# Kernel tuning notes

Measured on AMD Instinct MI355X. Metric: run time of the kernel, lower is better.

Reference implementation:

```python
import jax, jax.numpy as jnp
import numpy as np

UNITS = 256
INNER_ITERS = 1
INNER_LR = [0.01]
LN_EPS = 1e-3  # keras LayerNormalization default epsilon
B, L, F = 512, 128, 128


def _encoder(W1, b1, W2, b2, z):
    # keras 'gelu' activation is exact (approximate=False)
    h = jax.nn.gelu(z @ W1 + b1, approximate=False)
    return h @ W2 + b2


def _layer_norm(z, g, b):
    m = jnp.mean(z, axis=-1, keepdims=True)
    v = jnp.var(z, axis=-1, keepdims=True)
    return g * (z - m) / jnp.sqrt(v + LN_EPS) + b


def setup_inputs():
    U = UNITS
    key = jax.random.key(0)
    ks = jax.random.split(key, 12)
    s = 0.02
    return {
        "inputs": jax.random.normal(ks[0], (B, F), jnp.float32),
        "prev_hidden": jax.random.normal(ks[1], (B, U), jnp.float32),
        "sequence_buffer": jax.random.normal(ks[2], (B, L, U), jnp.float32),
        "Wp": jax.random.normal(ks[3], (F, U)) * s, "bp": jnp.zeros((U,)),
        "Wphi": jax.random.normal(ks[4], (U, U)) * s, "bphi": jnp.zeros((U,)),
        "Wpsi": jax.random.normal(ks[5], (U, U)) * s, "bpsi": jnp.zeros((U,)),
        "W1": jax.random.normal(ks[6], (U, 4 * U)) * s, "b1": jnp.zeros((4 * U,)),
        "W2": jax.random.normal(ks[7], (4 * U, U)) * s, "b2": jnp.zeros((U,)),
        "Wg": jax.random.normal(ks[8], (U, U)) * s, "g_bias": jnp.zeros((U,)),
        "ln_g": jnp.ones((U,)), "ln_b": jnp.zeros((U,)),
        "Wh": jax.random.normal(ks[9], (U, U)) * s, "h_bias": jnp.zeros((U,)),
    }


def reference(inputs, prev_hidden, sequence_buffer, Wp, bp, Wphi, bphi, Wpsi, bpsi,
              W1, b1, W2, b2, Wg, g_bias, ln_g, ln_b, Wh, h_bias):
    U = UNITS
    bsz = inputs.shape[0]
    # input projection (F != units)
    proj = inputs @ Wp + bp                                   # [B, U]
    # shift buffer, append projected input
    buf = jnp.concatenate([sequence_buffer[:, 1:, :], proj[:, None, :]], axis=1)  # [B, L, U]
    x = buf[:, :-1, :].reshape(-1, U)                         # [B*(L-1), U]
    y = buf[:, 1:, :].reshape(-1, U)
    phi = x @ Wphi + bphi

    params = (W1, b1, W2, b2)

    def inner_loss(p):
        rec = _layer_norm(_encoder(*p, phi) @ Wg + g_bias, ln_g, ln_b)
        return jnp.mean(jnp.square(rec - y)), rec

    rec = None
    for it in range(INNER_ITERS):
        (_, rec), grads = jax.value_and_grad(inner_loss, has_aux=True)(params)
        lr = INNER_LR[min(it, len(INNER_LR) - 1)]
        params = tuple(p - lr * g for p, g in zip(params, grads))

    psi = buf[:, -1, :] @ Wpsi + bpsi                         # [B, U]
    contrib = jnp.mean(rec.reshape(bsz, -1, U), axis=1)       # [B, U]
    # psi path uses the UPDATED inner-encoder weights
    out = (_encoder(*params, psi) + contrib) @ Wh + h_bias    # [B, U]
    return out, buf
```

## Files before the change

### kernel.cpp

```cpp
#include <hip/hip_runtime.h>
#include <cmath>

typedef __bf16 bf16;
typedef __attribute__((ext_vector_type(8))) __bf16 bf16x8;
typedef __attribute__((ext_vector_type(4))) __bf16 bf16x4v;
typedef __attribute__((ext_vector_type(4))) float f32x4;
typedef __attribute__((ext_vector_type(2))) unsigned int u32x2;

constexpr int NROWS = 512 * 127;
constexpr float LR = 0.01f;
constexpr float INV_NU = 1.f / (65024.f * 256.f);

__device__ __forceinline__ float sigf(float x) {
  return 1.f / (1.f + __expf(-1.702f * x));
}
__device__ __forceinline__ float gelu_fast(float x) { return x * sigf(x); }
__device__ __forceinline__ float dgelu_fast(float x) {
  float s = sigf(x);
  return s * (1.f + 1.702f * x * (1.f - s));
}
__device__ __forceinline__ bf16x8 gelu8f(bf16x8 v) {
  bf16x8 o;
#pragma unroll
  for (int i = 0; i < 8; i++) o[i] = (bf16)gelu_fast((float)v[i]);
  return o;
}

__device__ __forceinline__ void gload16(const bf16* g, const bf16* lds) {
  __builtin_amdgcn_global_load_lds(
      (const __attribute__((address_space(1))) unsigned int*)(size_t)(const void*)g,
      (__attribute__((address_space(3))) unsigned int*)(unsigned)(size_t)(const void*)lds,
      16, 0, 0);
}

__device__ __forceinline__ int xcd_lin() {
  int p = ((int)blockIdx.z * (int)gridDim.y + (int)blockIdx.y) * (int)gridDim.x + (int)blockIdx.x;
  const int total = (int)gridDim.x * (int)gridDim.y * (int)gridDim.z;
  if (!(total & 7)) p = (p & 7) * (total >> 3) + (p >> 3);
  return p;
}

template <int EPI>
__global__ __launch_bounds__(256) void gemm3_k(
    const bf16* __restrict__ A, const bf16* __restrict__ Bt,
    const float* __restrict__ bias, void* __restrict__ out0,
    void* __restrict__ out1, const bf16* __restrict__ aux,
    int M, int N, int K) {
  __shared__ __align__(16) bf16 As[2][128 * 64];
  __shared__ __align__(16) bf16 Bs[2][128 * 64];
  const int t = threadIdx.x;
  const int p = xcd_lin();
  const int bn = (p % (int)gridDim.x) * 128;
  const int bm = (p / (int)gridDim.x) * 128;
  const int lane = t & 63, w = t >> 6;
  const int wr = w >> 1, wc = w & 1;

  f32x4 acc[4][4];
#pragma unroll
  for (int mi = 0; mi < 4; mi++)
#pragma unroll
    for (int ni = 0; ni < 4; ni++) {
      f32x4 z = {0.f, 0.f, 0.f, 0.f};
      acc[mi][ni] = z;
    }

  const int l8 = lane >> 3;
  const int pp = lane & 7;
  const int csw = pp ^ l8;
  const bf16* aBase = A + (size_t)(bm + 32 * w + l8) * K + csw * 8;
  const bf16* bBase = Bt + (size_t)(bn + 32 * w + l8) * K + csw * 8;

  const int ml = lane & 15, g = lane >> 4;
  const int c0 = g ^ (ml & 7);
  const int c1 = (4 | g) ^ (ml & 7);

  const int nt = K >> 6;
#pragma unroll
  for (int i = 0; i < 4; i++) {
    gload16(aBase + (size_t)(8 * i) * K, As[0] + (32 * w + 8 * i) * 64);
    gload16(bBase + (size_t)(8 * i) * K, Bs[0] + (32 * w + 8 * i) * 64);
  }

  for (int tt = 0; tt < nt; tt++) {
    const int cur = tt & 1;
    if (tt + 1 < nt) {
      const int ko = (tt + 1) * 64;
#pragma unroll
      for (int i = 0; i < 4; i++) {
        gload16(aBase + (size_t)(8 * i) * K + ko, As[cur ^ 1] + (32 * w + 8 * i) * 64);
        gload16(bBase + (size_t)(8 * i) * K + ko, Bs[cur ^ 1] + (32 * w + 8 * i) * 64);
      }
      asm volatile("s_waitcnt vmcnt(8)" ::: "memory");
    } else {
      asm volatile("s_waitcnt vmcnt(0)" ::: "memory");
    }
    __builtin_amdgcn_s_barrier();
    __builtin_amdgcn_sched_barrier(0);

    bf16x8 af[2][4], bfr[2][4];
#pragma unroll
    for (int mi = 0; mi < 4; mi++) {
      const int m = wr * 64 + mi * 16 + ml;
      const int n = wc * 64 + mi * 16 + ml;
      af[0][mi] = *(const bf16x8*)&As[cur][m * 64 + c0 * 8];
      af[1][mi] = *(const bf16x8*)&As[cur][m * 64 + c1 * 8];
      bfr[0][mi] = *(const bf16x8*)&Bs[cur][n * 64 + c0 * 8];
      bfr[1][mi] = *(const bf16x8*)&Bs[cur][n * 64 + c1 * 8];
    }
#pragma unroll
    for (int ks = 0; ks < 2; ks++)
#pragma unroll
      for (int mi = 0; mi < 4; mi++)
#pragma unroll
        for (int ni = 0; ni < 4; ni++)
          acc[mi][ni] = __builtin_amdgcn_mfma_f32_16x16x32_bf16(
              bfr[ks][ni], af[ks][mi], acc[mi][ni], 0, 0, 0);
    __builtin_amdgcn_s_barrier();
  }

  const int g4 = (lane >> 4) << 2;
#pragma unroll
  for (int mi = 0; mi < 4; mi++) {
    const int m = bm + wr * 64 + mi * 16 + ml;
#pragma unroll
    for (int ni = 0; ni < 4; ni++) {
      const int n0 = bn + wc * 64 + ni * 16 + g4;
      f32x4 v = acc[mi][ni];
      if (bias) {
        const float4 bv = *(const float4*)(bias + n0);
        v[0] += bv.x; v[1] += bv.y; v[2] += bv.z; v[3] += bv.w;
      }
      const size_t idx = (size_t)m * N + n0;
      if constexpr (EPI == 0) {
        *(float4*)((float*)out0 + idx) = make_float4(v[0], v[1], v[2], v[3]);
      } else if constexpr (EPI == 1) {
        bf16x4v o;
#pragma unroll
        for (int j = 0; j < 4; j++) o[j] = (bf16)v[j];
        *(bf16x4v*)((bf16*)out0 + idx) = o;
      } else if constexpr (EPI == 2) {
        bf16x4v od, oh;
#pragma unroll
        for (int j = 0; j < 4; j++) {
          float s = sigf(v[j]);
          oh[j] = (bf16)(v[j] * s);
          od[j] = (bf16)(s * (1.f + 1.702f * v[j] * (1.f - s)));
        }
        *(bf16x4v*)((bf16*)out0 + idx) = od;
        *(bf16x4v*)((bf16*)out1 + idx) = oh;
      } else if constexpr (EPI == 3) {
        bf16x4v o;
#pragma unroll
        for (int j = 0; j < 4; j++) o[j] = (bf16)gelu_fast(v[j]);
        *(bf16x4v*)((bf16*)out0 + idx) = o;
      } else if constexpr (EPI == 5) {
        const bf16x4v a4 = *(const bf16x4v*)(aux + idx);
        bf16x4v o;
#pragma unroll
        for (int j = 0; j < 4; j++) o[j] = (bf16)(v[j] * dgelu_fast((float)a4[j]));
        *(bf16x4v*)((bf16*)out0 + idx) = o;
      } else {
        const bf16x4v a4 = *(const bf16x4v*)(aux + idx);
        bf16x4v o;
#pragma unroll
        for (int j = 0; j < 4; j++) o[j] = (bf16)(v[j] * (float)a4[j]);
        *(bf16x4v*)((bf16*)out0 + idx) = o;
      }
    }
  }
}

template <int EPI, bool GA>
__global__ __launch_bounds__(256) void gemm_k(
    const bf16* __restrict__ A, const bf16* __restrict__ Bt,
    const float* __restrict__ bias, void* __restrict__ out0,
    void* __restrict__ out1, const bf16* __restrict__ aux,
    int M, int N, int K) {
  __shared__ bf16 As[128][40];
  __shared__ bf16 Bs[128][40];
  const int t = threadIdx.x;
  const int bm = blockIdx.x * 128, bn = blockIdx.y * 128;
  const int lane = t & 63, w = t >> 6;
  const int wr = w >> 1, wc = w & 1;

  f32x4 acc[4][4];
#pragma unroll
  for (int mi = 0; mi < 4; mi++)
#pragma unroll
    for (int ni = 0; ni < 4; ni++) {
      f32x4 z = {0.f, 0.f, 0.f, 0.f};
      acc[mi][ni] = z;
    }
  const int r2 = t >> 2;
  const int c8 = (t & 3) * 8;

  for (int kt = 0; kt < K; kt += 32) {
    __syncthreads();
    {
      bf16x8 a0 = *(const bf16x8*)(A + (size_t)(bm + r2) * K + kt + c8);
      bf16x8 a1 = *(const bf16x8*)(A + (size_t)(bm + r2 + 64) * K + kt + c8);
      bf16x8 b0 = *(const bf16x8*)(Bt + (size_t)(bn + r2) * K + kt + c8);
      bf16x8 b1 = *(const bf16x8*)(Bt + (size_t)(bn + r2 + 64) * K + kt + c8);
      if constexpr (GA) { a0 = gelu8f(a0); a1 = gelu8f(a1); }
      *(bf16x8*)&As[r2][c8] = a0;
      *(bf16x8*)&As[r2 + 64][c8] = a1;
      *(bf16x8*)&Bs[r2][c8] = b0;
      *(bf16x8*)&Bs[r2 + 64][c8] = b1;
    }
    __syncthreads();
    bf16x8 af[4], bfr[4];
#pragma unroll
    for (int mi = 0; mi < 4; mi++)
      af[mi] = *(const bf16x8*)&As[wr * 64 + mi * 16 + (lane & 15)][(lane >> 4) * 8];
#pragma unroll
    for (int ni = 0; ni < 4; ni++)
      bfr[ni] = *(const bf16x8*)&Bs[wc * 64 + ni * 16 + (lane & 15)][(lane >> 4) * 8];
#pragma unroll
    for (int mi = 0; mi < 4; mi++)
#pragma unroll
      for (int ni = 0; ni < 4; ni++)
        acc[mi][ni] = __builtin_amdgcn_mfma_f32_16x16x32_bf16(af[mi], bfr[ni], acc[mi][ni], 0, 0, 0);
  }

#pragma unroll
  for (int ni = 0; ni < 4; ni++) {
    const int col = bn + wc * 64 + ni * 16 + (lane & 15);
    const float bv = bias ? bias[col] : 0.f;
#pragma unroll
    for (int mi = 0; mi < 4; mi++) {
      const int rb = bm + wr * 64 + mi * 16 + ((lane >> 4) << 2);
#pragma unroll
      for (int r = 0; r < 4; r++) {
        float v = acc[mi][ni][r] + bv;
        size_t idx = (size_t)(rb + r) * N + col;
        if constexpr (EPI == 1) {
          ((bf16*)out0)[idx] = (bf16)v;
        } else {
          ((float*)out0)[idx] = v;
        }
      }
    }
  }
}

template <bool GELU_A>
__global__ __launch_bounds__(256) void tgemm4_k(
    const bf16* __restrict__ Asrc, const bf16* __restrict__ Bsrc,
    float* __restrict__ outP, int M, int N, int ldA, int ldB, int K) {
  __shared__ __align__(16) bf16 As[2][4736];
  __shared__ __align__(16) bf16 Bs[2][4736];
  const int t = threadIdx.x;
  const int p = xcd_lin();
  const int gx = (int)gridDim.x, gy = (int)gridDim.y;
  const int bm = (p % gx) * 128;
  const int bn = ((p / gx) % gy) * 128;
  const int zc = p / (gx * gy);
  const int r0 = zc * 1024;
  const int rows = (K - r0 < 1024) ? (K - r0) : 1024;
  const int nt = rows >> 5;
  const int lane = t & 63, w = t >> 6, wr = w >> 1, wc = w & 1;

  f32x4 acc[4][4];
#pragma unroll
  for (int mi = 0; mi < 4; mi++)
#pragma unroll
    for (int ni = 0; ni < 4; ni++) {
      f32x4 z = {0.f, 0.f, 0.f, 0.f};
      acc[mi][ni] = z;
    }

  const bool isB = t >= 128;
  const int srow = (t & 127) >> 4;
  const int scol = (t & 15) * 8;
  const int sms = (t & 15) >> 1;
  const int shalf = (t & 1) * 8;
  const bf16* src = isB ? Bsrc : Asrc;
  const int ld = isB ? ldB : ldA;
  const int bx = isB ? bn : bm;
  const int sidx = sms * 592 + srow * 16 + shalf;

  const unsigned abase = (unsigned)(size_t)(void*)As;
  const unsigned bbase = (unsigned)(size_t)(void*)Bs;
  const int g = lane >> 4;
  const int ml = lane & 15;
  const unsigned acol0 = abase + 2u * (unsigned)((wr * 4) * 592 + g * 144 + ml);
  const unsigned bcol0 = bbase + 2u * (unsigned)((wc * 4) * 592 + g * 144 + ml);

  auto ldrow = [&](int kt, int ll) {
    return *(const bf16x8*)(src + (size_t)(r0 + kt + srow + ll * 8) * ld + bx + scol);
  };
  auto wrbuf = [&](bf16* dst, bf16x8* stg) {
#pragma unroll
    for (int ll = 0; ll < 4; ll++) {
      bf16x8 v = stg[ll];
      if constexpr (GELU_A) { if (!isB) v = gelu8f(v); }
      *(bf16x8*)&dst[sidx + ll * 144] = v;
    }
  };

  bf16x8 stg[4];
#pragma unroll
  for (int ll = 0; ll < 4; ll++) stg[ll] = ldrow(0, ll);
  wrbuf(isB ? Bs[0] : As[0], stg);
  __syncthreads();

  for (int tt = 0; tt < nt; tt++) {
    const int cur = tt & 1;
    if (tt + 1 < nt) {
#pragma unroll
      for (int ll = 0; ll < 4; ll++) stg[ll] = ldrow((tt + 1) * 32, ll);
    }
    const unsigned boff = (unsigned)cur * (4736u * 2u);
    union FR { u32x2 pr[2]; bf16x8 v; };
    FR af[4], bfr[4];
#pragma unroll
    for (int mi = 0; mi < 4; mi++) {
      const unsigned a = acol0 + boff + (unsigned)(mi * 1184);
      asm volatile("ds_read_b64_tr_b16 %0, %1" : "=v"(af[mi].pr[0]) : "v"(a));
      asm volatile("ds_read_b64_tr_b16 %0, %1 offset:128" : "=v"(af[mi].pr[1]) : "v"(a));
    }
#pragma unroll
    for (int ni = 0; ni < 4; ni++) {
      const unsigned b = bcol0 + boff + (unsigned)(ni * 1184);
      asm volatile("ds_read_b64_tr_b16 %0, %1" : "=v"(bfr[ni].pr[0]) : "v"(b));
      asm volatile("ds_read_b64_tr_b16 %0, %1 offset:128" : "=v"(bfr[ni].pr[1]) : "v"(b));
    }
    asm volatile("s_waitcnt lgkmcnt(0)" ::: "memory");
    __builtin_amdgcn_sched_barrier(0);

#pragma unroll
    for (int mi = 0; mi < 4; mi++)
#pragma unroll
      for (int ni = 0; ni < 4; ni++)
        acc[mi][ni] = __builtin_amdgcn_mfma_f32_16x16x32_bf16(
            bfr[ni].v, af[mi].v, acc[mi][ni], 0, 0, 0);

    if (tt + 1 < nt) wrbuf(isB ? Bs[cur ^ 1] : As[cur ^ 1], stg);
    __syncthreads();
  }

  float* o = outP + (size_t)zc * M * N;
  const int g4 = (lane >> 4) << 2;
#pragma unroll
  for (int mi = 0; mi < 4; mi++) {
    const int m = bm + wr * 64 + mi * 16 + ml;
#pragma unroll
    for (int ni = 0; ni < 4; ni++) {
      const int n0 = bn + wc * 64 + ni * 16 + g4;
      f32x4 v = acc[mi][ni];
      *(float4*)(o + (size_t)m * N + n0) = make_float4(v[0], v[1], v[2], v[3]);
    }
  }
}

__global__ void prep_k(const float* inputs, const float* Wp, const float* Wphi,
                       const float* W1, const float* W2, const float* Wg,
                       const float* Wpsi, const float* Wh,
                       bf16* inb, bf16* WpT, bf16* WphiT, bf16* W1T, bf16* W2T,
                       bf16* WgT, bf16* Wgb, bf16* W2b, bf16* WpsiT, bf16* WhT) {
  int i = blockIdx.x * 256 + threadIdx.x;
  if (i < 65536) {
    inb[i] = (bf16)inputs[i];
  } else if ((i -= 65536) < 32768) {
    int u = i >> 7, f = i & 127;
    WpT[i] = (bf16)Wp[f * 256 + u];
  } else if ((i -= 32768) < 65536) {
    int n = i >> 8, k = i & 255;
    WphiT[i] = (bf16)Wphi[k * 256 + n];
  } else if ((i -= 65536) < 262144) {
    int h = i >> 8, u = i & 255;
    W1T[i] = (bf16)W1[u * 1024 + h];
  } else if ((i -= 262144) < 262144) {
    int u = i >> 10, h = i & 1023;
    W2T[i] = (bf16)W2[h * 256 + u];
  } else if ((i -= 262144) < 65536) {
    int n = i >> 8, k = i & 255;
    WgT[i] = (bf16)Wg[k * 256 + n];
  } else if ((i -= 65536) < 65536) {
    Wgb[i] = (bf16)Wg[i];
  } else if ((i -= 65536) < 262144) {
    W2b[i] = (bf16)W2[i];
  } else if ((i -= 262144) < 65536) {
    int n = i >> 8, k = i & 255;
    WpsiT[i] = (bf16)Wpsi[k * 256 + n];
  } else if ((i -= 65536) < 65536) {
    int n = i >> 8, k = i & 255;
    WhT[i] = (bf16)Wh[k * 256 + n];
  }
}

__global__ void bzg_k(const float* __restrict__ b2, const float* __restrict__ Wg,
                      const float* __restrict__ gbias, float* __restrict__ bzg) {
  const int n = threadIdx.x;
  float s = gbias[n];
  for (int j = 0; j < 256; j++) s += b2[j] * Wg[j * 256 + n];
  bzg[n] = s;
}

__global__ void xcast_k(const float* __restrict__ seq, bf16* __restrict__ xb) {
  int v8 = blockIdx.x * 256 + threadIdx.x;
  int r = v8 >> 5, c8 = (v8 & 31) * 8;
  int b = r / 127, t = r - b * 127;
  const float* src = seq + ((size_t)(b * 128 + t + 1)) * 256 + c8;
  float4 v0 = *(const float4*)(src);
  float4 v1 = *(const float4*)(src + 4);
  bf16x8 o;
  o[0] = (bf16)v0.x; o[1] = (bf16)v0.y; o[2] = (bf16)v0.z; o[3] = (bf16)v0.w;
  o[4] = (bf16)v1.x; o[5] = (bf16)v1.y; o[6] = (bf16)v1.z; o[7] = (bf16)v1.w;
  *(bf16x8*)(xb + (size_t)r * 256 + c8) = o;
}

__global__ void projcast_k(const float* __restrict__ proj, bf16* __restrict__ projb) {
  int i = blockIdx.x * 256 + threadIdx.x;
  projb[i] = (bf16)proj[i];
}

__global__ void bufwrite_k(const float* __restrict__ seq, const float* __restrict__ proj,
                           float* __restrict__ buf) {
  int i = blockIdx.x * 256 + threadIdx.x;
  int b = i >> 13, rem = i & 8191;
  int j = rem >> 6, c4 = (rem & 63) * 4;
  float4 v;
  if (j < 127)
    v = *(const float4*)(seq + ((size_t)(b * 128 + j + 1)) * 256 + c4);
  else
    v = *(const float4*)(proj + (size_t)b * 256 + c4);
  *(float4*)(buf + ((size_t)(b * 128 + j)) * 256 + c4) = v;
}

__global__ __launch_bounds__(256) void ln_k(const bf16* zin, bf16* dzout,
                                            const float* __restrict__ seq,
                                            const float* __restrict__ proj,
                                            const float* __restrict__ lng,
                                            const float* __restrict__ lnb,
                                            bf16* __restrict__ rec) {
  const int w = threadIdx.x >> 6, lane = threadIdx.x & 63;
  const int r = blockIdx.x * 4 + w;
  const int b = r / 127, tt = r - b * 127;
  typedef __attribute__((ext_vector_type(4))) __bf16 bf16x4;
  bf16x4 zv = *(const bf16x4*)(zin + (size_t)r * 256 + lane * 4);
  float z0 = (float)zv[0], z1 = (float)zv[1], z2 = (float)zv[2], z3 = (float)zv[3];
  float s1 = z0 + z1 + z2 + z3;
  float s2 = z0 * z0 + z1 * z1 + z2 * z2 + z3 * z3;
  for (int m = 1; m < 64; m <<= 1) { s1 += __shfl_xor(s1, m); s2 += __shfl_xor(s2, m); }
  const float mean = s1 * (1.f / 256.f);
  const float var = s2 * (1.f / 256.f) - mean * mean;
  const float rs = rsqrtf(var + 1e-3f);
  const float4 gv = *(const float4*)(lng + lane * 4);
  const float4 bv = *(const float4*)(lnb + lane * 4);
  const float* ysrc = (tt < 126) ? (seq + ((size_t)(b * 128 + tt + 2)) * 256)
                                 : (proj + (size_t)b * 256);
  const float4 yv = *(const float4*)(ysrc + lane * 4);
  float xh0 = (z0 - mean) * rs, xh1 = (z1 - mean) * rs, xh2 = (z2 - mean) * rs, xh3 = (z3 - mean) * rs;
  float r0 = gv.x * xh0 + bv.x, r1 = gv.y * xh1 + bv.y, r2 = gv.z * xh2 + bv.z, r3 = gv.w * xh3 + bv.w;
  float u0 = 2.f * (r0 - yv.x) * INV_NU * gv.x;
  float u1 = 2.f * (r1 - yv.y) * INV_NU * gv.y;
  float u2 = 2.f * (r2 - yv.z) * INV_NU * gv.z;
  float u3 = 2.f * (r3 - yv.w) * INV_NU * gv.w;
  float t1 = u0 + u1 + u2 + u3;
  float t2 = u0 * xh0 + u1 * xh1 + u2 * xh2 + u3 * xh3;
  for (int m = 1; m < 64; m <<= 1) { t1 += __shfl_xor(t1, m); t2 += __shfl_xor(t2, m); }
  const float mu = t1 * (1.f / 256.f), mux = t2 * (1.f / 256.f);
  bf16x4 ro, dzo;
  ro[0] = (bf16)r0; ro[1] = (bf16)r1; ro[2] = (bf16)r2; ro[3] = (bf16)r3;
  dzo[0] = (bf16)((u0 - mu - xh0 * mux) * rs);
  dzo[1] = (bf16)((u1 - mu - xh1 * mux) * rs);
  dzo[2] = (bf16)((u2 - mu - xh2 * mux) * rs);
  dzo[3] = (bf16)((u3 - mu - xh3 * mux) * rs);
  *(bf16x4*)(rec + (size_t)r * 256 + lane * 4) = ro;
  *(bf16x4*)(dzout + (size_t)r * 256 + lane * 4) = dzo;
}

__global__ void colsum_k(const bf16* __restrict__ src, float* __restrict__ part, int C) {
  const int col = blockIdx.x * 256 + threadIdx.x;
  const int ch = blockIdx.y;
  float s = 0.f;
  const int rbeg = ch * 1016;
  for (int rr = rbeg; rr < rbeg + 1016; rr++) s += (float)src[(size_t)rr * C + col];
  part[(size_t)ch * C + col] = s;
}

__global__ void contrib_k(const bf16* __restrict__ rec, float* __restrict__ contrib) {
  const int b = blockIdx.x, u = threadIdx.x;
  float s = 0.f;
  for (int t = 0; t < 127; t++) s += (float)rec[((size_t)b * 127 + t) * 256 + u];
  contrib[b * 256 + u] = s * (1.f / 127.f);
}

__global__ void update2_k(const float* __restrict__ pW2, const float* __restrict__ pdb2,
                          const float* __restrict__ W2, const float* __restrict__ b2,
                          bf16* __restrict__ W2pT, float* __restrict__ b2p) {
  int idx = blockIdx.x * 256 + threadIdx.x;
  if (idx < 262144) {
    float s = 0.f;
    for (int z = 0; z < 64; z++) s += pW2[(size_t)z * 262144 + idx];
    int h = idx >> 8, u = idx & 255;
    W2pT[(size_t)u * 1024 + h] = (bf16)(W2[idx] - LR * s);
  } else {
    int u = idx - 262144;
    float s = 0.f;
    for (int c = 0; c < 64; c++) s += pdb2[c * 256 + u];
    b2p[u] = b2[u] - LR * s;
  }
}

__global__ void update1_k(const float* __restrict__ pW1, const float* __restrict__ pdb1,
                          const float* __restrict__ W1, const float* __restrict__ b1,
                          bf16* __restrict__ W1pT, float* __restrict__ b1p) {
  int idx = blockIdx.x * 256 + threadIdx.x;
  if (idx < 262144) {
    float s = 0.f;
    for (int z = 0; z < 64; z++) s += pW1[(size_t)z * 262144 + idx];
    int u = idx >> 10, h = idx & 1023;
    W1pT[(size_t)h * 256 + u] = (bf16)(W1[idx] - LR * s);
  } else {
    int h = idx - 262144;
    float s = 0.f;
    for (int c = 0; c < 64; c++) s += pdb1[c * 1024 + h];
    b1p[h] = b1[h] - LR * s;
  }
}

__global__ void fin_k(const float* __restrict__ encp, const float* __restrict__ contrib,
                      bf16* __restrict__ fin) {
  int i = blockIdx.x * 256 + threadIdx.x;
  fin[i] = (bf16)(encp[i] + contrib[i]);
}

extern "C" void kernel_launch(void* const* d_in, const int* in_sizes, int n_in,
                              void* d_out, int out_size, void* d_ws, size_t ws_size,
                              hipStream_t stream) {
  const float* inputs = (const float*)d_in[0];
  const float* seq = (const float*)d_in[2];
  const float* Wp = (const float*)d_in[3];
  const float* bp = (const float*)d_in[4];
  const float* Wphi = (const float*)d_in[5];
  const float* bphi = (const float*)d_in[6];
  const float* Wpsi = (const float*)d_in[7];
  const float* bpsi = (const float*)d_in[8];
  const float* W1 = (const float*)d_in[9];
  const float* b1 = (const float*)d_in[10];
  const float* W2 = (const float*)d_in[11];
  const float* b2 = (const float*)d_in[12];
  const float* Wg = (const float*)d_in[13];
  const float* gbias = (const float*)d_in[14];
  const float* lng = (const float*)d_in[15];
  const float* lnb = (const float*)d_in[16];
  const float* Wh = (const float*)d_in[17];
  const float* hbias = (const float*)d_in[18];

  float* out = (float*)d_out;
  float* buf = out + 131072;
  float* pW2 = buf;
  float* pW1 = buf;

  char* wptr = (char*)d_ws;
  auto alloc = [&](size_t bytes) {
    char* p = wptr;
    wptr += (bytes + 255) & ~(size_t)255;
    return p;
  };
  bf16* inb   = (bf16*)alloc(65536 * 2);
  bf16* WpT   = (bf16*)alloc(32768 * 2);
  bf16* WphiT = (bf16*)alloc(65536 * 2);
  bf16* W1T   = (bf16*)alloc(262144 * 2);
  bf16* W2T   = (bf16*)alloc(262144 * 2);
  bf16* WgT   = (bf16*)alloc(65536 * 2);
  bf16* Wgb   = (bf16*)alloc(65536 * 2);
  bf16* W2b   = (bf16*)alloc(262144 * 2);
  bf16* WpsiT = (bf16*)alloc(65536 * 2);
  bf16* WhT   = (bf16*)alloc(65536 * 2);
  bf16* WzgT  = (bf16*)alloc(262144 * 2);
  float* bzg  = (float*)alloc(256 * 4);
  bf16* W1pT  = (bf16*)alloc(262144 * 2);
  bf16* W2pT  = (bf16*)alloc(262144 * 2);
  float* b1p  = (float*)alloc(1024 * 4);
  float* b2p  = (float*)alloc(256 * 4);
  float* proj = (float*)alloc(131072 * 4);
  bf16* projb = (bf16*)alloc(131072 * 2);
  float* pdb2 = (float*)alloc(64 * 256 * 4);
  float* pdb1 = (float*)alloc(64 * 1024 * 4);
  bf16* psib  = (bf16*)alloc(131072 * 2);
  bf16* hpb   = (bf16*)alloc(524288 * 2);
  float* encp = (float*)alloc(131072 * 4);
  float* contrib = (float*)alloc(131072 * 4);
  bf16* finb  = (bf16*)alloc(131072 * 2);
  const size_t NU = (size_t)NROWS * 256;
  const size_t NH = (size_t)NROWS * 1024;
  bf16* xz     = (bf16*)alloc(NU * 2);
  bf16* phi    = (bf16*)alloc(NU * 2);
  bf16* a1b    = (bf16*)alloc(NH * 2);
  bf16* encden = (bf16*)alloc(NU * 2);
  const bool useH = ws_size >= (size_t)((char*)wptr - (char*)d_ws) + NH * 2 + 4096;
  bf16* hbuf = useH ? (bf16*)alloc(NH * 2) : nullptr;

  prep_k<<<4736, 256, 0, stream>>>(inputs, Wp, Wphi, W1, W2, Wg, Wpsi, Wh,
                                   inb, WpT, WphiT, W1T, W2T, WgT, Wgb, W2b, WpsiT, WhT);
  gemm3_k<1><<<dim3(8, 2), 256, 0, stream>>>(WgT, W2b, nullptr, WzgT, nullptr, nullptr, 256, 1024, 256);
  bzg_k<<<1, 256, 0, stream>>>(b2, Wg, gbias, bzg);
  xcast_k<<<8128, 256, 0, stream>>>(seq, xz);
  gemm3_k<0><<<dim3(2, 4), 256, 0, stream>>>(inb, WpT, bp, proj, nullptr, nullptr, 512, 256, 128);
  projcast_k<<<512, 256, 0, stream>>>(proj, projb);
  gemm3_k<1><<<dim3(2, 508), 256, 0, stream>>>(xz, WphiT, bphi, phi, nullptr, nullptr, NROWS, 256, 256);
  if (useH)
    gemm3_k<2><<<dim3(8, 508), 256, 0, stream>>>(phi, W1T, b1, a1b, hbuf, nullptr, NROWS, 1024, 256);
  else
    gemm3_k<1><<<dim3(8, 508), 256, 0, stream>>>(phi, W1T, b1, a1b, nullptr, nullptr, NROWS, 1024, 256);
  if (useH)
    gemm3_k<1><<<dim3(2, 508), 256, 0, stream>>>(hbuf, WzgT, bzg, xz, nullptr, nullptr, NROWS, 256, 1024);
  else
    gemm_k<1, true><<<dim3(508, 2), 256, 0, stream>>>(a1b, WzgT, bzg, xz, nullptr, nullptr, NROWS, 256, 1024);
  ln_k<<<16256, 256, 0, stream>>>(xz, xz, seq, proj, lng, lnb, encden);
  contrib_k<<<512, 256, 0, stream>>>(encden, contrib);
  gemm3_k<1><<<dim3(2, 508), 256, 0, stream>>>(xz, Wgb, nullptr, encden, nullptr, nullptr, NROWS, 256, 256);
  colsum_k<<<dim3(1, 64), 256, 0, stream>>>(encden, pdb2, 256);
  if (useH)
    tgemm4_k<false><<<dim3(8, 2, 64), 256, 0, stream>>>(hbuf, encden, pW2, 1024, 256, 1024, 256, NROWS);
  else
    tgemm4_k<true><<<dim3(8, 2, 64), 256, 0, stream>>>(a1b, encden, pW2, 1024, 256, 1024, 256, NROWS);
  update2_k<<<1025, 256, 0, stream>>>(pW2, pdb2, W2, b2, W2pT, b2p);
  if (useH)
    gemm3_k<6><<<dim3(8, 508), 256, 0, stream>>>(encden, W2b, nullptr, a1b, nullptr, a1b, NROWS, 1024, 256);
  else
    gemm3_k<5><<<dim3(8, 508), 256, 0, stream>>>(encden, W2b, nullptr, a1b, nullptr, a1b, NROWS, 1024, 256);
  colsum_k<<<dim3(4, 64), 256, 0, stream>>>(a1b, pdb1, 1024);
  tgemm4_k<false><<<dim3(2, 8, 64), 256, 0, stream>>>(phi, a1b, pW1, 256, 1024, 256, 1024, NROWS);
  update1_k<<<1028, 256, 0, stream>>>(pW1, pdb1, W1, b1, W1pT, b1p);
  bufwrite_k<<<16384, 256, 0, stream>>>(seq, proj, buf);
  gemm3_k<1><<<dim3(2, 4), 256, 0, stream>>>(projb, WpsiT, bpsi, psib, nullptr, nullptr, 512, 256, 256);
  gemm3_k<3><<<dim3(8, 4), 256, 0, stream>>>(psib, W1pT, b1p, hpb, nullptr, nullptr, 512, 1024, 256);
  gemm3_k<0><<<dim3(2, 4), 256, 0, stream>>>(hpb, W2pT, b2p, encp, nullptr, nullptr, 512, 256, 1024);
  fin_k<<<512, 256, 0, stream>>>(encp, contrib, finb);
  gemm3_k<0><<<dim3(2, 4), 256, 0, stream>>>(finb, WhT, hbias, out, nullptr, nullptr, 512, 256, 256);
}
```

Measured before the change: 904.5 us.

## Recompute GELU in GEMM A-load, drop hbuf, fuse small casts and halve split-K

Drops the extra gelu(h) buffer, which was written by the W1 GEMM. The Wzg GEMM now applies GELU to the A fragments after the LDS read in the pipelined gemm3 kernel, and the backward pass recomputes dgelu from a1b. Two small elementwise kernels are removed: the proj bf16 cast is folded into the proj GEMM epilogue, and the contrib add into the W2 GEMM epilogue. The weight-gradient split-K goes from 64 to 32 chunks of 2048 rows, which shrinks the partial buffers and the reduction work. The cost is extra GELU ALU work inside the K loop and less parallelism in the weight-gradient GEMMs.

```diff
diff --git a/kernel.cpp b/kernel.cpp
--- a/kernel.cpp
+++ b/kernel.cpp
@@ -40,7 +40,7 @@
   return p;
 }
 
-template <int EPI>
+template <int EPI, bool GLA>
 __global__ __launch_bounds__(256) void gemm3_k(
     const bf16* __restrict__ A, const bf16* __restrict__ Bt,
     const float* __restrict__ bias, void* __restrict__ out0,
@@ -104,6 +104,7 @@
       const int n = wc * 64 + mi * 16 + ml;
       af[0][mi] = *(const bf16x8*)&As[cur][m * 64 + c0 * 8];
       af[1][mi] = *(const bf16x8*)&As[cur][m * 64 + c1 * 8];
+      if constexpr (GLA) { af[0][mi] = gelu8f(af[0][mi]); af[1][mi] = gelu8f(af[1][mi]); }
       bfr[0][mi] = *(const bf16x8*)&Bs[cur][n * 64 + c0 * 8];
       bfr[1][mi] = *(const bf16x8*)&Bs[cur][n * 64 + c1 * 8];
     }
@@ -138,16 +139,6 @@
 #pragma unroll
         for (int j = 0; j < 4; j++) o[j] = (bf16)v[j];
         *(bf16x4v*)((bf16*)out0 + idx) = o;
-      } else if constexpr (EPI == 2) {
-        bf16x4v od, oh;
-#pragma unroll
-        for (int j = 0; j < 4; j++) {
-          float s = sigf(v[j]);
-          oh[j] = (bf16)(v[j] * s);
-          od[j] = (bf16)(s * (1.f + 1.702f * v[j] * (1.f - s)));
-        }
-        *(bf16x4v*)((bf16*)out0 + idx) = od;
-        *(bf16x4v*)((bf16*)out1 + idx) = oh;
       } else if constexpr (EPI == 3) {
         bf16x4v o;
 #pragma unroll
@@ -159,85 +150,18 @@
 #pragma unroll
         for (int j = 0; j < 4; j++) o[j] = (bf16)(v[j] * dgelu_fast((float)a4[j]));
         *(bf16x4v*)((bf16*)out0 + idx) = o;
+      } else if constexpr (EPI == 7) {
+        *(float4*)((float*)out0 + idx) = make_float4(v[0], v[1], v[2], v[3]);
+        bf16x4v o;
+#pragma unroll
+        for (int j = 0; j < 4; j++) o[j] = (bf16)v[j];
+        *(bf16x4v*)((bf16*)out1 + idx) = o;
       } else {
-        const bf16x4v a4 = *(const bf16x4v*)(aux + idx);
+        const float4 c4 = *(const float4*)((const float*)aux + idx);
         bf16x4v o;
-#pragma unroll
-        for (int j = 0; j < 4; j++) o[j] = (bf16)(v[j] * (float)a4[j]);
+        o[0] = (bf16)(v[0] + c4.x); o[1] = (bf16)(v[1] + c4.y);
+        o[2] = (bf16)(v[2] + c4.z); o[3] = (bf16)(v[3] + c4.w);
         *(bf16x4v*)((bf16*)out0 + idx) = o;
-      }
-    }
-  }
-}
-
-template <int EPI, bool GA>
-__global__ __launch_bounds__(256) void gemm_k(
-    const bf16* __restrict__ A, const bf16* __restrict__ Bt,
-    const float* __restrict__ bias, void* __restrict__ out0,
-    void* __restrict__ out1, const bf16* __restrict__ aux,
-    int M, int N, int K) {
-  __shared__ bf16 As[128][40];
-  __shared__ bf16 Bs[128][40];
-  const int t = threadIdx.x;
-  const int bm = blockIdx.x * 128, bn = blockIdx.y * 128;
-  const int lane = t & 63, w = t >> 6;
-  const int wr = w >> 1, wc = w & 1;
-
-  f32x4 acc[4][4];
-#pragma unroll
-  for (int mi = 0; mi < 4; mi++)
-#pragma unroll
-    for (int ni = 0; ni < 4; ni++) {
-      f32x4 z = {0.f, 0.f, 0.f, 0.f};
-      acc[mi][ni] = z;
-    }
-  const int r2 = t >> 2;
-  const int c8 = (t & 3) * 8;
-
-  for (int kt = 0; kt < K; kt += 32) {
-    __syncthreads();
-    {
-      bf16x8 a0 = *(const bf16x8*)(A + (size_t)(bm + r2) * K + kt + c8);
-      bf16x8 a1 = *(const bf16x8*)(A + (size_t)(bm + r2 + 64) * K + kt + c8);
-      bf16x8 b0 = *(const bf16x8*)(Bt + (size_t)(bn + r2) * K + kt + c8);
-      bf16x8 b1 = *(const bf16x8*)(Bt + (size_t)(bn + r2 + 64) * K + kt + c8);
-      if constexpr (GA) { a0 = gelu8f(a0); a1 = gelu8f(a1); }
-      *(bf16x8*)&As[r2][c8] = a0;
-      *(bf16x8*)&As[r2 + 64][c8] = a1;
-      *(bf16x8*)&Bs[r2][c8] = b0;
-      *(bf16x8*)&Bs[r2 + 64][c8] = b1;
-    }
-    __syncthreads();
-    bf16x8 af[4], bfr[4];
-#pragma unroll
-    for (int mi = 0; mi < 4; mi++)
-      af[mi] = *(const bf16x8*)&As[wr * 64 + mi * 16 + (lane & 15)][(lane >> 4) * 8];
-#pragma unroll
-    for (int ni = 0; ni < 4; ni++)
-      bfr[ni] = *(const bf16x8*)&Bs[wc * 64 + ni * 16 + (lane & 15)][(lane >> 4) * 8];
-#pragma unroll
-    for (int mi = 0; mi < 4; mi++)
-#pragma unroll
-      for (int ni = 0; ni < 4; ni++)
-        acc[mi][ni] = __builtin_amdgcn_mfma_f32_16x16x32_bf16(af[mi], bfr[ni], acc[mi][ni], 0, 0, 0);
-  }
-
-#pragma unroll
-  for (int ni = 0; ni < 4; ni++) {
-    const int col = bn + wc * 64 + ni * 16 + (lane & 15);
-    const float bv = bias ? bias[col] : 0.f;
-#pragma unroll
-    for (int mi = 0; mi < 4; mi++) {
-      const int rb = bm + wr * 64 + mi * 16 + ((lane >> 4) << 2);
-#pragma unroll
-      for (int r = 0; r < 4; r++) {
-        float v = acc[mi][ni][r] + bv;
-        size_t idx = (size_t)(rb + r) * N + col;
-        if constexpr (EPI == 1) {
-          ((bf16*)out0)[idx] = (bf16)v;
-        } else {
-          ((float*)out0)[idx] = v;
-        }
       }
     }
   }
@@ -255,8 +179,8 @@
   const int bm = (p % gx) * 128;
   const int bn = ((p / gx) % gy) * 128;
   const int zc = p / (gx * gy);
-  const int r0 = zc * 1024;
-  const int rows = (K - r0 < 1024) ? (K - r0) : 1024;
+  const int r0 = zc * 2048;
+  const int rows = (K - r0 < 2048) ? (K - r0) : 2048;
   const int nt = rows >> 5;
   const int lane = t & 63, w = t >> 6, wr = w >> 1, wc = w & 1;
 
@@ -408,11 +332,6 @@
   o[0] = (bf16)v0.x; o[1] = (bf16)v0.y; o[2] = (bf16)v0.z; o[3] = (bf16)v0.w;
   o[4] = (bf16)v1.x; o[5] = (bf16)v1.y; o[6] = (bf16)v1.z; o[7] = (bf16)v1.w;
   *(bf16x8*)(xb + (size_t)r * 256 + c8) = o;
-}
-
-__global__ void projcast_k(const float* __restrict__ proj, bf16* __restrict__ projb) {
-  int i = blockIdx.x * 256 + threadIdx.x;
-  projb[i] = (bf16)proj[i];
 }
 
 __global__ void bufwrite_k(const float* __restrict__ seq, const float* __restrict__ proj,
@@ -493,7 +412,7 @@
   int idx = blockIdx.x * 256 + threadIdx.x;
   if (idx < 262144) {
     float s = 0.f;
-    for (int z = 0; z < 64; z++) s += pW2[(size_t)z * 262144 + idx];
+    for (int z = 0; z < 32; z++) s += pW2[(size_t)z * 262144 + idx];
     int h = idx >> 8, u = idx & 255;
     W2pT[(size_t)u * 1024 + h] = (bf16)(W2[idx] - LR * s);
   } else {
@@ -510,7 +429,7 @@
   int idx = blockIdx.x * 256 + threadIdx.x;
   if (idx < 262144) {
     float s = 0.f;
-    for (int z = 0; z < 64; z++) s += pW1[(size_t)z * 262144 + idx];
+    for (int z = 0; z < 32; z++) s += pW1[(size_t)z * 262144 + idx];
     int u = idx >> 10, h = idx & 1023;
     W1pT[(size_t)h * 256 + u] = (bf16)(W1[idx] - LR * s);
   } else {
@@ -519,12 +438,6 @@
     for (int c = 0; c < 64; c++) s += pdb1[c * 1024 + h];
     b1p[h] = b1[h] - LR * s;
   }
-}
-
-__global__ void fin_k(const float* __restrict__ encp, const float* __restrict__ contrib,
-                      bf16* __restrict__ fin) {
-  int i = blockIdx.x * 256 + threadIdx.x;
-  fin[i] = (bf16)(encp[i] + contrib[i]);
 }
 
 extern "C" void kernel_launch(void* const* d_in, const int* in_sizes, int n_in,
@@ -591,45 +504,29 @@
   bf16* phi    = (bf16*)alloc(NU * 2);
   bf16* a1b    = (bf16*)alloc(NH * 2);
   bf16* encden = (bf16*)alloc(NU * 2);
-  const bool useH = ws_size >= (size_t)((char*)wptr - (char*)d_ws) + NH * 2 + 4096;
-  bf16* hbuf = useH ? (bf16*)alloc(NH * 2) : nullptr;
 
   prep_k<<<4736, 256, 0, stream>>>(inputs, Wp, Wphi, W1, W2, Wg, Wpsi, Wh,
                                    inb, WpT, WphiT, W1T, W2T, WgT, Wgb, W2b, WpsiT, WhT);
-  gemm3_k<1><<<dim3(8, 2), 256, 0, stream>>>(WgT, W2b, nullptr, WzgT, nullptr, nullptr, 256, 1024, 256);
+  gemm3_k<1, false><<<dim3(8, 2), 256, 0, stream>>>(WgT, W2b, nullptr, WzgT, nullptr, nullptr, 256, 1024, 256);
   bzg_k<<<1, 256, 0, stream>>>(b2, Wg, gbias, bzg);
   xcast_k<<<8128, 256, 0, stream>>>(seq, xz);
-  gemm3_k<0><<<dim3(2, 4), 256, 0, stream>>>(inb, WpT, bp, proj, nullptr, nullptr, 512, 256, 128);
-  projcast_k<<<512, 256, 0, stream>>>(proj, projb);
-  gemm3_k<1><<<dim3(2, 508), 256, 0, stream>>>(xz, WphiT, bphi, phi, nullptr, nullptr, NROWS, 256, 256);
-  if (useH)
-    gemm3_k<2><<<dim3(8, 508), 256, 0, stream>>>(phi, W1T, b1, a1b, hbuf, nullptr, NROWS, 1024, 256);
-  else
-    gemm3_k<1><<<dim3(8, 508), 256, 0, stream>>>(phi, W1T, b1, a1b, nullptr, nullptr, NROWS, 1024, 256);
-  if (useH)
-    gemm3_k<1><<<dim3(2, 508), 256, 0, stream>>>(hbuf, WzgT, bzg, xz, nullptr, nullptr, NROWS, 256, 1024);
-  else
-    gemm_k<1, true><<<dim3(508, 2), 256, 0, stream>>>(a1b, WzgT, bzg, xz, nullptr, nullptr, NROWS, 256, 1024);
+  gemm3_k<7, false><<<dim3(2, 4), 256, 0, stream>>>(inb, WpT, bp, proj, projb, nullptr, 512, 256, 128);
+  gemm3_k<1, false><<<dim3(2, 508), 256, 0, stream>>>(xz, WphiT, bphi, phi, nullptr, nullptr, NROWS, 256, 256);
+  gemm3_k<1, false><<<dim3(8, 508), 256, 0, stream>>>(phi, W1T, b1, a1b, nullptr, nullptr, NROWS, 1024, 256);
+  gemm3_k<1, true><<<dim3(2, 508), 256, 0, stream>>>(a1b, WzgT, bzg, xz, nullptr, nullptr, NROWS, 256, 1024);
   ln_k<<<16256, 256, 0, stream>>>(xz, xz, seq, proj, lng, lnb, encden);
   contrib_k<<<512, 256, 0, stream>>>(encden, contrib);
-  gemm3_k<1><<<dim3(2, 508), 256, 0, stream>>>(xz, Wgb, nullptr, encden, nullptr, nullptr, NROWS, 256, 256);
+  gemm3_k<1, false><<<dim3(2, 508), 256, 0, stream>>>(xz, Wgb, nullptr, encden, nullptr, nullptr, NROWS, 256, 256);
   colsum_k<<<dim3(1, 64), 256, 0, stream>>>(encden, pdb2, 256);
-  if (useH)
-    tgemm4_k<false><<<dim3(8, 2, 64), 256, 0, stream>>>(hbuf, encden, pW2, 1024, 256, 1024, 256, NROWS);
-  else
-    tgemm4_k<true><<<dim3(8, 2, 64), 256, 0, stream>>>(a1b, encden, pW2, 1024, 256, 1024, 256, NROWS);
+  tgemm4_k<true><<<dim3(8, 2, 32), 256, 0, stream>>>(a1b, encden, pW2, 1024, 256, 1024, 256, NROWS);
   update2_k<<<1025, 256, 0, stream>>>(pW2, pdb2, W2, b2, W2pT, b2p);
-  if (useH)
-    gemm3_k<6><<<dim3(8, 508), 256, 0, stream>>>(encden, W2b, nullptr, a1b, nullptr, a1b, NROWS, 1024, 256);
-  else
-    gemm3_k<5><<<dim3(8, 508), 256, 0, stream>>>(encden, W2b, nullptr, a1b, nullptr, a1b, NROWS, 1024, 256);
+  gemm3_k<5, false><<<dim3(8, 508), 256, 0, stream>>>(encden, W2b, nullptr, a1b, nullptr, a1b, NROWS, 1024, 256);
   colsum_k<<<dim3(4, 64), 256, 0, stream>>>(a1b, pdb1, 1024);
-  tgemm4_k<false><<<dim3(2, 8, 64), 256, 0, stream>>>(phi, a1b, pW1, 256, 1024, 256, 1024, NROWS);
+  tgemm4_k<false><<<dim3(2, 8, 32), 256, 0, stream>>>(phi, a1b, pW1, 256, 1024, 256, 1024, NROWS);
   update1_k<<<1028, 256, 0, stream>>>(pW1, pdb1, W1, b1, W1pT, b1p);
   bufwrite_k<<<16384, 256, 0, stream>>>(seq, proj, buf);
-  gemm3_k<1><<<dim3(2, 4), 256, 0, stream>>>(projb, WpsiT, bpsi, psib, nullptr, nullptr, 512, 256, 256);
-  gemm3_k<3><<<dim3(8, 4), 256, 0, stream>>>(psib, W1pT, b1p, hpb, nullptr, nullptr, 512, 1024, 256);
-  gemm3_k<0><<<dim3(2, 4), 256, 0, stream>>>(hpb, W2pT, b2p, encp, nullptr, nullptr, 512, 256, 1024);
-  fin_k<<<512, 256, 0, stream>>>(encp, contrib, finb);
-  gemm3_k<0><<<dim3(2, 4), 256, 0, stream>>>(finb, WhT, hbias, out, nullptr, nullptr, 512, 256, 256);
-}
+  gemm3_k<1, false><<<dim3(2, 4), 256, 0, stream>>>(projb, WpsiT, bpsi, psib, nullptr, nullptr, 512, 256, 256);
+  gemm3_k<3, false><<<dim3(8, 4), 256, 0, stream>>>(psib, W1pT, b1p, hpb, nullptr, nullptr, 512, 1024, 256);
+  gemm3_k<8, false><<<dim3(2, 4), 256, 0, stream>>>(hpb, W2pT, b2p, finb, nullptr, (const bf16*)contrib, 512, 256, 1024);
+  gemm3_k<0, false><<<dim3(2, 4), 256, 0, stream>>>(finb, WhT, hbias, out, nullptr, nullptr, 512, 256, 256);
+}
```

Result: slower. 1.005 ms (+11.1%).
